# Kernel optimization log

Hardware: AMD Instinct MI355X
Metric: run time of the kernel (lower is better)

Reference implementation:

```python
import jax, jax.numpy as jnp
import numpy as np

D_STATE = 16
DT_RANK = 48
D_CONV = 4
EPS = 1e-5


def rmsnorm(x, w):
    return x * jax.lax.rsqrt(jnp.mean(x * x, axis=-1, keepdims=True) + EPS) * w


def causal_dw_conv(u, w, b):
    # u: [B,T,D], w: [D,K] depthwise causal kernel, b: [D]
    B, T, D = u.shape
    K = w.shape[1]
    up = jnp.pad(u, ((0, 0), (K - 1, 0), (0, 0)))
    acc = jnp.zeros_like(u)
    for k in range(K):  # K=4, tiny fixed loop
        acc = acc + up[:, k:k + T, :] * w[:, k]
    return acc + b


def mamba_mixer(h, ipw, cw, cb, xpw, dpw, dpb, alog, dpar, opw):
    # h: [B,T,d_model]
    B, T, _ = h.shape
    xz = h @ ipw.T                       # [B,T,2*d_inner]
    u, z = jnp.split(xz, 2, axis=-1)     # each [B,T,d_inner]
    u = jax.nn.silu(causal_dw_conv(u, cw, cb))
    xp = u @ xpw.T                       # [B,T,dt_rank+2*d_state]
    dt = xp[..., :DT_RANK]
    Bm = xp[..., DT_RANK:DT_RANK + D_STATE]
    Cm = xp[..., DT_RANK + D_STATE:]
    delta = jax.nn.softplus(dt @ dpw.T + dpb)      # [B,T,d_inner]
    A = -jnp.exp(alog)                              # [d_inner, d_state], negative
    dA = jnp.exp(delta[..., None] * A)              # [B,T,d_inner,d_state] in (0,1)
    dBu = (delta * u)[..., None] * Bm[:, :, None, :]
    # time-major for scan
    dA_t = jnp.moveaxis(dA, 1, 0)
    dBu_t = jnp.moveaxis(dBu, 1, 0)
    C_t = jnp.moveaxis(Cm, 1, 0)

    def step(hst, inp):
        a, bu, c = inp
        hst = a * hst + bu                          # [B,d_inner,d_state]
        y = jnp.einsum('bdn,bn->bd', hst, c)
        return hst, y

    h0 = jnp.zeros((B, u.shape[-1], D_STATE), u.dtype)
    _, ys = jax.lax.scan(step, h0, (dA_t, dBu_t, C_t))
    y = jnp.moveaxis(ys, 0, 1) + u * dpar           # skip via D
    y = y * jax.nn.silu(z)                          # gate
    return y @ opw.T                                # [B,T,d_model]


def setup_inputs() -> dict:
    key = jax.random.key(0)
    ks = jax.random.split(key, 16)
    L, d_model, d_inner = 4, 768, 1536
    B, C, T = 4, 256, 512
    s = 0.02
    return {
        'x': jax.random.normal(ks[0], (B, C, T), jnp.float32),
        'in_proj_w': jax.random.normal(ks[1], (L, 2 * d_inner, d_model), jnp.float32) * s,
        'conv_w': jax.random.normal(ks[2], (L, d_inner, D_CONV), jnp.float32) * 0.3,
        'conv_b': jnp.zeros((L, d_inner), jnp.float32),
        'x_proj_w': jax.random.normal(ks[3], (L, DT_RANK + 2 * D_STATE, d_inner), jnp.float32) * s,
        'dt_proj_w': jax.random.normal(ks[4], (L, d_inner, DT_RANK), jnp.float32) * 0.1,
        'dt_proj_b': jax.random.normal(ks[5], (L, d_inner), jnp.float32) * 0.1 - 4.0,
        'A_log': jax.random.uniform(ks[6], (L, d_inner, D_STATE), jnp.float32, 0.0, 1.5),
        'D_param': jax.random.uniform(ks[7], (L, d_inner), jnp.float32),
        'out_proj_w': jax.random.normal(ks[8], (L, d_model, d_inner), jnp.float32) * s,
        'norm_w': jnp.ones((L, d_model), jnp.float32),
        'norm_f_w': jnp.ones((d_model,), jnp.float32),
        'inp_w': jax.random.normal(ks[9], (d_model, C), jnp.float32) * s,
        'inp_b': jnp.zeros((d_model,), jnp.float32),
        'cls_w': jax.random.normal(ks[10], (10, d_model), jnp.float32) * s,
        'cls_b': jnp.zeros((10,), jnp.float32),
    }


def reference(x, in_proj_w, conv_w, conv_b, x_proj_w, dt_proj_w, dt_proj_b,
              A_log, D_param, out_proj_w, norm_w, norm_f_w,
              inp_w, inp_b, cls_w, cls_b):
    # x: (B, C, T) -> (B, T, C)
    xt = jnp.transpose(x, (0, 2, 1))
    h = xt @ inp_w.T + inp_b                # [B,T,d_model]
    hidden = h
    residual = None
    L = in_proj_w.shape[0]
    for l in range(L):
        residual = hidden if residual is None else hidden + residual
        normed = rmsnorm(residual, norm_w[l])
        hidden = mamba_mixer(normed, in_proj_w[l], conv_w[l], conv_b[l],
                             x_proj_w[l], dt_proj_w[l], dt_proj_b[l],
                             A_log[l], D_param[l], out_proj_w[l])
    residual = hidden + residual
    hidden = rmsnorm(residual, norm_f_w)
    pooled = hidden.mean(axis=1)            # [B,d_model]
    logits = pooled @ cls_w.T + cls_b       # [B,num_labels]
    return logits
```

## Files before the change

### kernel.cpp

```cpp
#include <hip/hip_runtime.h>
#include <math.h>

#define D_MODEL 768
#define D_INNER 1536
#define B_SZ 4
#define T_SZ 512
#define ROWS (B_SZ*T_SZ)
#define XP_N 80
#define CH 32
#define CT 16
#define XS 8
#define XKC (D_INNER/XS)
#define OS 4
#define OKC (D_INNER/OS)
#define MN_OUT (ROWS*768)

typedef __attribute__((ext_vector_type(8))) short bf16x8;
typedef __attribute__((ext_vector_type(4))) float f32x4;

#define GLL(g, l) __builtin_amdgcn_global_load_lds( \
    (const __attribute__((address_space(1))) void*)(g), \
    (__attribute__((address_space(3))) void*)(l), 16, 0, 0)

__device__ __forceinline__ float sigmoidf_(float x){ return 1.0f/(1.0f+__expf(-x)); }
__device__ __forceinline__ float siluf_(float x){ return x*sigmoidf_(x); }
__device__ __forceinline__ unsigned short f2bf(float f){
  unsigned u = __builtin_bit_cast(unsigned, f);
  u = (u + 0x7FFFu + ((u >> 16) & 1u)) >> 16;
  return (unsigned short)u;
}

__global__ __launch_bounds__(256) void gemm_bf16(
    const unsigned short* __restrict__ A, const unsigned short* __restrict__ Wb,
    float* __restrict__ C, int M, int N, int K)
{
  __shared__ unsigned short As[2][64*32];
  __shared__ unsigned short Ws[2][128*32];
  const int tid = threadIdx.x;
  const int bm = blockIdx.y*64, bn = blockIdx.x*128;
  const int wave = tid >> 6, lane = tid & 63;
  const int wn = wave*32;
  const int fr = lane & 15, quad = lane >> 4;
  f32x4 acc[4][2] = {};
  const int chunk = wave*64 + lane;
  const int row0 = chunk >> 2;
  const int khp  = chunk & 3;
  const int khl  = (khp + 4 - ((row0 >> 1) & 3)) & 3;
  const unsigned short* Ag = A  + (size_t)(bm + row0)*K + khl*8;
  const unsigned short* Wg = Wb + (size_t)(bn + row0)*K + khl*8;
  const size_t rstep = (size_t)64*K;
  const int wo = wave*512;

  GLL(Ag,         As[0] + wo);
  GLL(Wg,         Ws[0] + wo);
  GLL(Wg + rstep, Ws[0] + wo + 2048);
  asm volatile("s_waitcnt vmcnt(0)" ::: "memory");
  __builtin_amdgcn_sched_barrier(0);
  __builtin_amdgcn_s_barrier();

  int cur = 0;
  for (int k0 = 0; k0 < K; k0 += 32){
    const int nxt = cur ^ 1;
    if (k0 + 32 < K){
      GLL(Ag + k0 + 32,         As[nxt] + wo);
      GLL(Wg + k0 + 32,         Ws[nxt] + wo);
      GLL(Wg + rstep + k0 + 32, Ws[nxt] + wo + 2048);
    }
    bf16x8 a[4], b[2];
    #pragma unroll
    for (int i=0;i<4;i++){
      const int row = i*16 + fr;
      a[i] = *(const bf16x8*)(As[cur] + row*32 + (((quad + (row>>1)) & 3)*8));
    }
    #pragma unroll
    for (int j=0;j<2;j++){
      const int row = wn + j*16 + fr;
      b[j] = *(const bf16x8*)(Ws[cur] + row*32 + (((quad + (row>>1)) & 3)*8));
    }
    #pragma unroll
    for (int i=0;i<4;i++)
      #pragma unroll
      for (int j=0;j<2;j++)
        acc[i][j] = __builtin_amdgcn_mfma_f32_16x16x32_bf16(a[i], b[j], acc[i][j], 0, 0, 0);
    asm volatile("s_waitcnt vmcnt(0)" ::: "memory");
    __builtin_amdgcn_sched_barrier(0);
    __builtin_amdgcn_s_barrier();
    cur = nxt;
  }
  #pragma unroll
  for (int i=0;i<4;i++){
    #pragma unroll
    for (int r=0;r<4;r++){
      const int row = bm + i*16 + quad*4 + r;
      float* Cp = C + (size_t)row*N + bn + wn + fr;
      #pragma unroll
      for (int j=0;j<2;j++)
        Cp[j*16] = acc[i][j][r];
    }
  }
}

__global__ __launch_bounds__(256) void gemm_bf16_sk(
    const unsigned short* __restrict__ A, const unsigned short* __restrict__ Wb,
    float* __restrict__ P0, float* __restrict__ P1, int M, int N, int K)
{
  __shared__ unsigned short As[2][64*32];
  __shared__ unsigned short Ws[2][128*32];
  const int tid = threadIdx.x;
  const int bm = blockIdx.y*64, bn = blockIdx.x*128;
  const int s = blockIdx.z;
  const int koff = s*OKC;
  const int wave = tid >> 6, lane = tid & 63;
  const int wn = wave*32;
  const int fr = lane & 15, quad = lane >> 4;
  f32x4 acc[4][2] = {};
  const int chunk = wave*64 + lane;
  const int row0 = chunk >> 2;
  const int khp  = chunk & 3;
  const int khl  = (khp + 4 - ((row0 >> 1) & 3)) & 3;
  const unsigned short* Ag = A  + (size_t)(bm + row0)*K + koff + khl*8;
  const unsigned short* Wg = Wb + (size_t)(bn + row0)*K + koff + khl*8;
  const size_t rstep = (size_t)64*K;
  const int wo = wave*512;

  GLL(Ag,         As[0] + wo);
  GLL(Wg,         Ws[0] + wo);
  GLL(Wg + rstep, Ws[0] + wo + 2048);
  asm volatile("s_waitcnt vmcnt(0)" ::: "memory");
  __builtin_amdgcn_sched_barrier(0);
  __builtin_amdgcn_s_barrier();

  int cur = 0;
  for (int k0 = 0; k0 < OKC; k0 += 32){
    const int nxt = cur ^ 1;
    if (k0 + 32 < OKC){
      GLL(Ag + k0 + 32,         As[nxt] + wo);
      GLL(Wg + k0 + 32,         Ws[nxt] + wo);
      GLL(Wg + rstep + k0 + 32, Ws[nxt] + wo + 2048);
    }
    bf16x8 a[4], b[2];
    #pragma unroll
    for (int i=0;i<4;i++){
      const int row = i*16 + fr;
      a[i] = *(const bf16x8*)(As[cur] + row*32 + (((quad + (row>>1)) & 3)*8));
    }
    #pragma unroll
    for (int j=0;j<2;j++){
      const int row = wn + j*16 + fr;
      b[j] = *(const bf16x8*)(Ws[cur] + row*32 + (((quad + (row>>1)) & 3)*8));
    }
    #pragma unroll
    for (int i=0;i<4;i++)
      #pragma unroll
      for (int j=0;j<2;j++)
        acc[i][j] = __builtin_amdgcn_mfma_f32_16x16x32_bf16(a[i], b[j], acc[i][j], 0, 0, 0);
    asm volatile("s_waitcnt vmcnt(0)" ::: "memory");
    __builtin_amdgcn_sched_barrier(0);
    __builtin_amdgcn_s_barrier();
    cur = nxt;
  }
  float* Cb = (s < 2 ? P0 : P1) + (size_t)(s & 1)*MN_OUT;
  #pragma unroll
  for (int i=0;i<4;i++){
    #pragma unroll
    for (int r=0;r<4;r++){
      const int row = bm + i*16 + quad*4 + r;
      float* Cp = Cb + (size_t)row*N + bn + wn + fr;
      #pragma unroll
      for (int j=0;j<2;j++)
        Cp[j*16] = acc[i][j][r];
    }
  }
}

__global__ __launch_bounds__(256) void sgemm_input(
    const float* __restrict__ x, const float* __restrict__ W,
    const float* __restrict__ bias, float* __restrict__ C)
{
  __shared__ float As[16][64];
  __shared__ float Wsh[16][64];
  const int bm = blockIdx.y*64, bn = blockIdx.x*64;
  const int b = bm >> 9, t0 = bm & (T_SZ-1);
  const int tid = threadIdx.x;
  const int tx = tid & 15, ty = tid >> 4;
  const int lm = tid & 63, lk = (tid >> 6) << 2;
  float acc[4][4] = {};
  const float* Wp = W + (size_t)(bn+lm)*256 + lk;
  const float* xb = x + ((size_t)b*256)*512 + t0 + lm;
  for (int k0 = 0; k0 < 256; k0 += 16){
    #pragma unroll
    for (int i=0;i<4;i++)
      As[lk+i][lm] = xb[(size_t)(k0+lk+i)*512];
    float4 wv = *(const float4*)(Wp + k0);
    Wsh[lk+0][lm]=wv.x; Wsh[lk+1][lm]=wv.y; Wsh[lk+2][lm]=wv.z; Wsh[lk+3][lm]=wv.w;
    __syncthreads();
    #pragma unroll
    for (int k = 0; k < 16; k++){
      float a[4], w[4];
      #pragma unroll
      for (int i=0;i<4;i++) a[i] = As[k][ty*4+i];
      #pragma unroll
      for (int j=0;j<4;j++) w[j] = Wsh[k][tx*4+j];
      #pragma unroll
      for (int i=0;i<4;i++)
        #pragma unroll
        for (int j=0;j<4;j++)
          acc[i][j] += a[i]*w[j];
    }
    __syncthreads();
  }
  #pragma unroll
  for (int i=0;i<4;i++){
    const int r = bm + ty*4 + i;
    #pragma unroll
    for (int j=0;j<4;j++){
      const int n = bn + tx*4 + j;
      C[(size_t)r*768 + n] = acc[i][j] + bias[n];
    }
  }
}

__global__ __launch_bounds__(256) void xproj_conv_splitk(
    const float* __restrict__ xz, const float* __restrict__ cw,
    const float* __restrict__ cb, const float* __restrict__ W,
    float* __restrict__ part)
{
  __shared__ float As[16][64];
  __shared__ float Wsh[16][80];
  const int bm = blockIdx.x*64;
  const int s = blockIdx.y;
  const int koff = s*XKC;
  const int tid = threadIdx.x;
  const int tx = tid & 15, ty = tid >> 4;
  const int lm = tid & 63, lk = (tid >> 6) << 2;
  float acc[4][5] = {};
  const int row = bm + lm;
  const int t = row & (T_SZ-1);
  for (int k0 = 0; k0 < XKC; k0 += 16){
    const int d0 = koff + k0 + lk;
    float4 cbv = *(const float4*)(cb + d0);
    float cba[4] = {cbv.x, cbv.y, cbv.z, cbv.w};
    float4 tp3 = *(const float4*)(xz + (size_t)row*3072 + d0);
    float4 tp0 = (t>=3) ? *(const float4*)(xz + (size_t)(row-3)*3072 + d0) : make_float4(0.f,0.f,0.f,0.f);
    float4 tp1 = (t>=2) ? *(const float4*)(xz + (size_t)(row-2)*3072 + d0) : make_float4(0.f,0.f,0.f,0.f);
    float4 tp2 = (t>=1) ? *(const float4*)(xz + (size_t)(row-1)*3072 + d0) : make_float4(0.f,0.f,0.f,0.f);
    float a0[4]={tp0.x,tp0.y,tp0.z,tp0.w}, a1[4]={tp1.x,tp1.y,tp1.z,tp1.w};
    float a2[4]={tp2.x,tp2.y,tp2.z,tp2.w}, a3[4]={tp3.x,tp3.y,tp3.z,tp3.w};
    #pragma unroll
    for (int i=0;i<4;i++){
      const float4 w4 = *(const float4*)(cw + (size_t)(d0+i)*4);
      float a = cba[i];
      a += a0[i]*w4.x; a += a1[i]*w4.y; a += a2[i]*w4.z; a += a3[i]*w4.w;
      As[lk+i][lm] = siluf_(a);
    }
    for (int i = tid; i < 320; i += 256){
      const int wr = i % 80, wk = (i / 80) << 2;
      float4 wv = *(const float4*)(W + (size_t)wr*D_INNER + koff + k0 + wk);
      Wsh[wk+0][wr]=wv.x; Wsh[wk+1][wr]=wv.y; Wsh[wk+2][wr]=wv.z; Wsh[wk+3][wr]=wv.w;
    }
    __syncthreads();
    #pragma unroll
    for (int k = 0; k < 16; k++){
      float a[4], w[5];
      #pragma unroll
      for (int i=0;i<4;i++) a[i] = As[k][ty*4+i];
      #pragma unroll
      for (int j=0;j<5;j++) w[j] = Wsh[k][tx*5+j];
      #pragma unroll
      for (int i=0;i<4;i++)
        #pragma unroll
        for (int j=0;j<5;j++)
          acc[i][j] += a[i]*w[j];
    }
    __syncthreads();
  }
  #pragma unroll
  for (int i=0;i<4;i++){
    const int r = bm + ty*4 + i;
    #pragma unroll
    for (int j=0;j<5;j++){
      const int n = tx*5 + j;
      part[((size_t)s*ROWS + r)*XP_N + n] = acc[i][j];
    }
  }
}

__global__ __launch_bounds__(256) void dtproj_fused(
    const float* __restrict__ part, const float* __restrict__ W,
    const float* __restrict__ bias, float* __restrict__ delta,
    float* __restrict__ xpbc)
{
  if (blockIdx.x >= 24){
    const int i = ((blockIdx.x - 24)*32 + blockIdx.y)*256 + threadIdx.x;
    const int r = i >> 5, cc = i & 31;
    float ssum = 0.f;
    #pragma unroll
    for (int s2=0;s2<XS;s2++)
      ssum += part[((size_t)s2*ROWS + r)*XP_N + 48 + cc];
    xpbc[(size_t)r*32 + cc] = ssum;
    return;
  }
  __shared__ float As[16][64];
  __shared__ float Wsh[16][64];
  const int bm = blockIdx.y*64, bn = blockIdx.x*64;
  const int tid = threadIdx.x;
  const int tx = tid & 15, ty = tid >> 4;
  const int lm = tid & 63, lk = (tid >> 6) << 2;
  float acc[4][4] = {};
  const float* Ap = part + (size_t)(bm+lm)*XP_N + lk;
  const float* Wp = W + (size_t)(bn+lm)*48 + lk;
  for (int k0 = 0; k0 < 48; k0 += 16){
    float4 av = make_float4(0.f,0.f,0.f,0.f);
    #pragma unroll
    for (int s2=0;s2<XS;s2++){
      const float4 pv = *(const float4*)(Ap + (size_t)s2*ROWS*XP_N + k0);
      av.x += pv.x; av.y += pv.y; av.z += pv.z; av.w += pv.w;
    }
    float4 wv = *(const float4*)(Wp + k0);
    As[lk+0][lm]=av.x; As[lk+1][lm]=av.y; As[lk+2][lm]=av.z; As[lk+3][lm]=av.w;
    Wsh[lk+0][lm]=wv.x; Wsh[lk+1][lm]=wv.y; Wsh[lk+2][lm]=wv.z; Wsh[lk+3][lm]=wv.w;
    __syncthreads();
    #pragma unroll
    for (int k = 0; k < 16; k++){
      float a[4], w[4];
      #pragma unroll
      for (int i=0;i<4;i++) a[i] = As[k][ty*4+i];
      #pragma unroll
      for (int j=0;j<4;j++) w[j] = Wsh[k][tx*4+j];
      #pragma unroll
      for (int i=0;i<4;i++)
        #pragma unroll
        for (int j=0;j<4;j++)
          acc[i][j] += a[i]*w[j];
    }
    __syncthreads();
  }
  #pragma unroll
  for (int i=0;i<4;i++){
    const int r = bm + ty*4 + i;
    #pragma unroll
    for (int j=0;j<4;j++){
      const int n = bn + tx*4 + j;
      float v = acc[i][j] + bias[n];
      v = (v > 20.f) ? v : log1pf(__expf(v));
      delta[(size_t)r*D_INNER + n] = v;
    }
  }
}

__global__ __launch_bounds__(256) void scan_pass1(
    const float* __restrict__ delta, const float* __restrict__ xz,
    const float* __restrict__ xpbc, const float* __restrict__ alog,
    const float* __restrict__ cw, const float* __restrict__ cb,
    float* __restrict__ Pend, float* __restrict__ Hend)
{
  const int d = blockIdx.x*256 + threadIdx.x;
  const int b = blockIdx.y, c = blockIdx.z;
  float4 t0 = *(const float4*)(alog + d*16 + 0);
  float4 t1 = *(const float4*)(alog + d*16 + 4);
  float4 t2 = *(const float4*)(alog + d*16 + 8);
  float4 t3 = *(const float4*)(alog + d*16 + 12);
  float Av[16] = {t0.x,t0.y,t0.z,t0.w,t1.x,t1.y,t1.z,t1.w,
                  t2.x,t2.y,t2.z,t2.w,t3.x,t3.y,t3.z,t3.w};
  float h[16];
  #pragma unroll
  for (int n=0;n<16;n++){ Av[n] = -__expf(Av[n]); h[n]=0.f; }
  float sdv = 0.f;
  const size_t row0 = (size_t)b*T_SZ + (size_t)c*CT;
  const float* dp  = delta + row0*D_INNER + d;
  const float* xp0 = xz    + row0*3072 + d;
  const float* bp  = xpbc  + row0*32;
  const float4 cwv = *(const float4*)(cw + (size_t)d*4);
  const float cbv = cb[d];
  float xm3, xm2, xm1;
  if (c == 0){ xm3 = xm2 = xm1 = 0.f; }
  else { xm3 = xp0[-3*3072]; xm2 = xp0[-2*3072]; xm1 = xp0[-1*3072]; }
  #pragma unroll 4
  for (int tt=0; tt<CT; tt++){
    const float dv = dp[(size_t)tt*D_INNER];
    const float xc = xp0[(size_t)tt*3072];
    float ua = cbv;
    ua += xm3*cwv.x; ua += xm2*cwv.y; ua += xm1*cwv.z; ua += xc*cwv.w;
    const float uv = siluf_(ua);
    xm3 = xm2; xm2 = xm1; xm1 = xc;
    const float4 B0 = *(const float4*)(bp + (size_t)tt*32);
    const float4 B1 = *(const float4*)(bp + (size_t)tt*32 + 4);
    const float4 B2 = *(const float4*)(bp + (size_t)tt*32 + 8);
    const float4 B3 = *(const float4*)(bp + (size_t)tt*32 + 12);
    const float Bv[16] = {B0.x,B0.y,B0.z,B0.w,B1.x,B1.y,B1.z,B1.w,
                          B2.x,B2.y,B2.z,B2.w,B3.x,B3.y,B3.z,B3.w};
    const float du = dv*uv;
    sdv += dv;
    #pragma unroll
    for (int n=0;n<16;n++){
      const float dA = __expf(dv*Av[n]);
      h[n] = dA*h[n] + du*Bv[n];
    }
  }
  float P[16];
  #pragma unroll
  for (int n=0;n<16;n++) P[n] = __expf(Av[n]*sdv);
  float* Pp = Pend + ((size_t)(b*CH+c)*D_INNER + d)*16;
  float* Hp = Hend + ((size_t)(b*CH+c)*D_INNER + d)*16;
  *(float4*)(Pp+ 0) = make_float4(P[0],P[1],P[2],P[3]);
  *(float4*)(Pp+ 4) = make_float4(P[4],P[5],P[6],P[7]);
  *(float4*)(Pp+ 8) = make_float4(P[8],P[9],P[10],P[11]);
  *(float4*)(Pp+12) = make_float4(P[12],P[13],P[14],P[15]);
  *(float4*)(Hp+ 0) = make_float4(h[0],h[1],h[2],h[3]);
  *(float4*)(Hp+ 4) = make_float4(h[4],h[5],h[6],h[7]);
  *(float4*)(Hp+ 8) = make_float4(h[8],h[9],h[10],h[11]);
  *(float4*)(Hp+12) = make_float4(h[12],h[13],h[14],h[15]);
}

__global__ __launch_bounds__(256) void scan_combine(
    const float* __restrict__ Pend, const float* __restrict__ Hend,
    float* __restrict__ Hin)
{
  const int gid = blockIdx.x*256 + threadIdx.x;
  const int b = gid / (D_INNER*16);
  const int r = gid % (D_INNER*16);
  const size_t base = (size_t)b*CH*D_INNER*16 + r;
  const size_t step = (size_t)D_INNER*16;
  float h = 0.f;
  Hin[base] = 0.f;
  #pragma unroll
  for (int c=0; c<CH-1; c++){
    h = Pend[base + (size_t)c*step]*h + Hend[base + (size_t)c*step];
    Hin[base + (size_t)(c+1)*step] = h;
  }
}

__global__ __launch_bounds__(256) void scan_pass3(
    const float* __restrict__ delta, const float* __restrict__ xz,
    const float* __restrict__ xpbc, const float* __restrict__ alog,
    const float* __restrict__ cw, const float* __restrict__ cb,
    const float* __restrict__ Dp, const float* __restrict__ Hin,
    unsigned short* __restrict__ yb)
{
  const int d = blockIdx.x*256 + threadIdx.x;
  const int b = blockIdx.y, c = blockIdx.z;
  float4 t0 = *(const float4*)(alog + d*16 + 0);
  float4 t1 = *(const float4*)(alog + d*16 + 4);
  float4 t2 = *(const float4*)(alog + d*16 + 8);
  float4 t3 = *(const float4*)(alog + d*16 + 12);
  float Av[16] = {t0.x,t0.y,t0.z,t0.w,t1.x,t1.y,t1.z,t1.w,
                  t2.x,t2.y,t2.z,t2.w,t3.x,t3.y,t3.z,t3.w};
  #pragma unroll
  for (int n=0;n<16;n++) Av[n] = -__expf(Av[n]);
  const float* Hp = Hin + ((size_t)(b*CH+c)*D_INNER + d)*16;
  float4 h0 = *(const float4*)(Hp+0);
  float4 h1 = *(const float4*)(Hp+4);
  float4 h2 = *(const float4*)(Hp+8);
  float4 h3 = *(const float4*)(Hp+12);
  float h[16] = {h0.x,h0.y,h0.z,h0.w,h1.x,h1.y,h1.z,h1.w,
                 h2.x,h2.y,h2.z,h2.w,h3.x,h3.y,h3.z,h3.w};
  const float Dv = Dp[d];
  const size_t row0 = (size_t)b*T_SZ + (size_t)c*CT;
  const float* dp  = delta + row0*D_INNER + d;
  const float* xp0 = xz    + row0*3072 + d;
  const float* zp  = xz    + row0*3072 + 1536 + d;
  const float* bp  = xpbc  + row0*32;
  unsigned short* yp = yb + row0*D_INNER + d;
  const float4 cwv = *(const float4*)(cw + (size_t)d*4);
  const float cbv = cb[d];
  float xm3, xm2, xm1;
  if (c == 0){ xm3 = xm2 = xm1 = 0.f; }
  else { xm3 = xp0[-3*3072]; xm2 = xp0[-2*3072]; xm1 = xp0[-1*3072]; }
  #pragma unroll 2
  for (int tt=0; tt<CT; tt++){
    const float dv = dp[(size_t)tt*D_INNER];
    const float xc = xp0[(size_t)tt*3072];
    const float zv = zp[(size_t)tt*3072];
    float ua = cbv;
    ua += xm3*cwv.x; ua += xm2*cwv.y; ua += xm1*cwv.z; ua += xc*cwv.w;
    const float uv = siluf_(ua);
    xm3 = xm2; xm2 = xm1; xm1 = xc;
    const float4 B0 = *(const float4*)(bp + (size_t)tt*32);
    const float4 B1 = *(const float4*)(bp + (size_t)tt*32 + 4);
    const float4 B2 = *(const float4*)(bp + (size_t)tt*32 + 8);
    const float4 B3 = *(const float4*)(bp + (size_t)tt*32 + 12);
    const float4 C0 = *(const float4*)(bp + (size_t)tt*32 + 16);
    const float4 C1 = *(const float4*)(bp + (size_t)tt*32 + 20);
    const float4 C2 = *(const float4*)(bp + (size_t)tt*32 + 24);
    const float4 C3 = *(const float4*)(bp + (size_t)tt*32 + 28);
    const float Bv[16] = {B0.x,B0.y,B0.z,B0.w,B1.x,B1.y,B1.z,B1.w,
                          B2.x,B2.y,B2.z,B2.w,B3.x,B3.y,B3.z,B3.w};
    const float Cv[16] = {C0.x,C0.y,C0.z,C0.w,C1.x,C1.y,C1.z,C1.w,
                          C2.x,C2.y,C2.z,C2.w,C3.x,C3.y,C3.z,C3.w};
    const float du = dv*uv;
    float pp = 0.f;
    #pragma unroll
    for (int n=0;n<16;n++){
      const float dA = __expf(dv*Av[n]);
      h[n] = dA*h[n] + du*Bv[n];
      pp += h[n]*Cv[n];
    }
    yp[(size_t)tt*D_INNER] = f2bf((pp + uv*Dv)*siluf_(zv));
  }
}

__global__ __launch_bounds__(256) void fused_norm_cast(
    float* __restrict__ resid, const float* __restrict__ P0, const float* __restrict__ P1,
    const float* __restrict__ w, unsigned short* __restrict__ obf, float* __restrict__ ofp,
    const float* __restrict__ cin1, unsigned short* __restrict__ co1, int cn1, int cnb1,
    const float* __restrict__ cin2, unsigned short* __restrict__ co2, int cn2)
{
  const int blk = blockIdx.x;
  if (blk >= 2048){
    const int cb = blk - 2048;
    const float* in; unsigned short* o; int i4;
    if (cb < cnb1){ in = cin1; o = co1; i4 = (cb*256 + threadIdx.x)*4; if (i4 >= cn1) return; }
    else { in = cin2; o = co2; i4 = ((cb-cnb1)*256 + threadIdx.x)*4; if (i4 >= cn2) return; }
    float4 v = *(const float4*)(in + i4);
    ushort4 r;
    r.x = f2bf(v.x); r.y = f2bf(v.y); r.z = f2bf(v.z); r.w = f2bf(v.w);
    *(ushort4*)(o + i4) = r;
    return;
  }
  const int row = blk;
  const int tid = threadIdx.x;
  float v[3];
  float ss = 0.f;
  #pragma unroll
  for (int i=0;i<3;i++){
    const int c = tid + i*256;
    const size_t idx = (size_t)row*768 + c;
    float r = resid[idx];
    if (P0) r += (P0[idx] + P0[MN_OUT + idx]) + (P1[idx] + P1[MN_OUT + idx]);
    v[i] = r;
    ss += r*r;
  }
  #pragma unroll
  for (int off=32; off>=1; off>>=1) ss += __shfl_xor(ss, off);
  __shared__ float sred[4];
  const int lane = tid & 63, wv = tid >> 6;
  if (lane == 0) sred[wv] = ss;
  __syncthreads();
  const float tot = sred[0]+sred[1]+sred[2]+sred[3];
  const float scale = rsqrtf(tot*(1.0f/768.0f) + 1e-5f);
  #pragma unroll
  for (int i=0;i<3;i++){
    const int c = tid + i*256;
    const size_t idx = (size_t)row*768 + c;
    if (P0) resid[idx] = v[i];
    const float o = v[i]*scale*w[c];
    if (obf) obf[idx] = f2bf(o);
    else     ofp[idx] = o;
  }
}

__global__ __launch_bounds__(256) void pool_partial(const float* __restrict__ normed,
                                                    float* __restrict__ part){
  const int i = blockIdx.x*256 + threadIdx.x;
  const int s = blockIdx.y;
  const int b = i / 768, m = i % 768;
  float sum = 0.f;
  const float* p = normed + ((size_t)b*T_SZ + s*32)*768 + m;
  #pragma unroll
  for (int t=0; t<32; t++) sum += p[(size_t)t*768];
  part[s*3072 + i] = sum;
}

__global__ __launch_bounds__(256) void pool_cls(const float* __restrict__ part,
                                                const float* __restrict__ cw,
                                                const float* __restrict__ cb,
                                                float* __restrict__ out){
  __shared__ float ls[768];
  const int b = blockIdx.x;
  const int tid = threadIdx.x;
  #pragma unroll
  for (int i=0;i<3;i++){
    const int m = tid + i*256;
    float s = 0.f;
    #pragma unroll
    for (int c=0;c<16;c++) s += part[c*3072 + b*768 + m];
    ls[m] = s * (1.0f/T_SZ);
  }
  __syncthreads();
  const int wave = tid >> 6, lane = tid & 63;
  for (int o = wave; o < 10; o += 4){
    float s = 0.f;
    for (int k = lane; k < 768; k += 64) s += ls[k]*cw[o*768 + k];
    #pragma unroll
    for (int off=32; off>=1; off>>=1) s += __shfl_xor(s, off);
    if (lane == 0) out[b*10 + o] = s + cb[o];
  }
}

extern "C" void kernel_launch(void* const* d_in, const int* in_sizes, int n_in,
                              void* d_out, int out_size, void* d_ws, size_t ws_size,
                              hipStream_t stream) {
  const float* x         = (const float*)d_in[0];
  const float* in_proj_w = (const float*)d_in[1];
  const float* conv_w    = (const float*)d_in[2];
  const float* conv_b    = (const float*)d_in[3];
  const float* x_proj_w  = (const float*)d_in[4];
  const float* dt_proj_w = (const float*)d_in[5];
  const float* dt_proj_b = (const float*)d_in[6];
  const float* A_log     = (const float*)d_in[7];
  const float* D_param   = (const float*)d_in[8];
  const float* out_proj_w= (const float*)d_in[9];
  const float* norm_w    = (const float*)d_in[10];
  const float* norm_f_w  = (const float*)d_in[11];
  const float* inp_w     = (const float*)d_in[12];
  const float* inp_b     = (const float*)d_in[13];
  const float* cls_w     = (const float*)d_in[14];
  const float* cls_b     = (const float*)d_in[15];
  float* out = (float*)d_out;

  char* ws = (char*)d_ws;
  auto carve = [&](size_t nelem)->float* {
    float* p = (float*)ws;
    ws += ((nelem*sizeof(float) + 255)/256)*256;
    return p;
  };
  float* resid  = carve((size_t)ROWS*768);
  float* normed = carve((size_t)ROWS*768);
  float* xz     = carve((size_t)ROWS*3072);
  float* ucv    = carve((size_t)ROWS*1536);
  float* xpbc   = carve((size_t)ROWS*32);
  float* delta  = carve((size_t)ROWS*1536);
  float* ybf_f  = carve((size_t)ROWS*1536/2);
  float* wbi_f  = carve((size_t)(3072*768)/2);
  float* wbo_f  = carve((size_t)(768*1536)/2);
  float* Pend   = carve((size_t)B_SZ*CH*D_INNER*16);
  float* Hend   = carve((size_t)B_SZ*CH*D_INNER*16);
  float* Hin    = carve((size_t)B_SZ*CH*D_INNER*16);
  float* xpart  = carve((size_t)XS*ROWS*XP_N);
  float* ppool  = carve((size_t)16*3072);

  unsigned short* normedb = (unsigned short*)normed;
  unsigned short* ybf = (unsigned short*)ybf_f;
  unsigned short* wbi = (unsigned short*)wbi_f;
  unsigned short* wbo = (unsigned short*)wbo_f;

  sgemm_input<<<dim3(12,32), 256, 0, stream>>>(x, inp_w, inp_b, resid);

  for (int l = 0; l < 4; l++){
    fused_norm_cast<<<2048 + 2304 + 1152, 256, 0, stream>>>(
        resid, l ? delta : nullptr, l ? ucv : nullptr,
        norm_w + (size_t)l*768, normedb, nullptr,
        in_proj_w + (size_t)l*3072*768, wbi, 3072*768, 2304,
        out_proj_w + (size_t)l*768*1536, wbo, 768*1536);
    gemm_bf16<<<dim3(24,32), 256, 0, stream>>>(normedb, wbi, xz, ROWS, 3072, 768);
    xproj_conv_splitk<<<dim3(32,XS), 256, 0, stream>>>(
        xz, conv_w + (size_t)l*1536*4, conv_b + (size_t)l*1536,
        x_proj_w + (size_t)l*XP_N*1536, xpart);
    dtproj_fused<<<dim3(32,32), 256, 0, stream>>>(
        xpart, dt_proj_w + (size_t)l*1536*48, dt_proj_b + (size_t)l*1536, delta, xpbc);
    scan_pass1<<<dim3(6,B_SZ,CH-1), 256, 0, stream>>>(
        delta, xz, xpbc, A_log + (size_t)l*1536*16,
        conv_w + (size_t)l*1536*4, conv_b + (size_t)l*1536, Pend, Hend);
    scan_combine<<<(B_SZ*D_INNER*16)/256, 256, 0, stream>>>(Pend, Hend, Hin);
    scan_pass3<<<dim3(6,B_SZ,CH), 256, 0, stream>>>(
        delta, xz, xpbc, A_log + (size_t)l*1536*16,
        conv_w + (size_t)l*1536*4, conv_b + (size_t)l*1536,
        D_param + (size_t)l*1536, Hin, ybf);
    gemm_bf16_sk<<<dim3(6,32,OS), 256, 0, stream>>>(ybf, wbo, delta, ucv, ROWS, 768, 1536);
  }

  fused_norm_cast<<<2048, 256, 0, stream>>>(
      resid, delta, ucv, norm_f_w, nullptr, normed,
      nullptr, nullptr, 0, 0, nullptr, nullptr, 0);
  pool_partial<<<dim3(12,16), 256, 0, stream>>>(normed, ppool);
  pool_cls<<<4, 256, 0, stream>>>(ppool, cls_w, cls_b, out);
}
```

Before: 813.9 us.

## Halve scan chunk count, shrink out-proj split-K, recompute chunk decay in combine

The chunked scan now uses 16 chunks of 32 timesteps instead of 32 of 16. The first pass stores only the per-channel delta sum instead of 16 decay products, and the combine kernel recomputes exp(A*sum) from A_log, which cuts the Pend write and read traffic. Out-proj split-K drops from 4 to 2, so the norm kernel sums two partial buffers instead of four. Fewer chunks mean a longer serial loop per thread and fewer blocks in the scan passes, and the lower split-K means fewer blocks in the out-proj GEMM.

```diff
diff --git a/kernel.cpp b/kernel.cpp
--- a/kernel.cpp
+++ b/kernel.cpp
@@ -7,11 +7,11 @@
 #define T_SZ 512
 #define ROWS (B_SZ*T_SZ)
 #define XP_N 80
-#define CH 32
-#define CT 16
+#define CH 16
+#define CT 32
 #define XS 8
 #define XKC (D_INNER/XS)
-#define OS 4
+#define OS 2
 #define OKC (D_INNER/OS)
 #define MN_OUT (ROWS*768)
 
@@ -159,7 +159,7 @@
     __builtin_amdgcn_s_barrier();
     cur = nxt;
   }
-  float* Cb = (s < 2 ? P0 : P1) + (size_t)(s & 1)*MN_OUT;
+  float* Cb = (s == 0 ? P0 : P1);
   #pragma unroll
   for (int i=0;i<4;i++){
     #pragma unroll
@@ -352,7 +352,7 @@
     const float* __restrict__ delta, const float* __restrict__ xz,
     const float* __restrict__ xpbc, const float* __restrict__ alog,
     const float* __restrict__ cw, const float* __restrict__ cb,
-    float* __restrict__ Pend, float* __restrict__ Hend)
+    float* __restrict__ sdvp, float* __restrict__ Hend)
 {
   const int d = blockIdx.x*256 + threadIdx.x;
   const int b = blockIdx.y, c = blockIdx.z;
@@ -397,15 +397,8 @@
       h[n] = dA*h[n] + du*Bv[n];
     }
   }
-  float P[16];
-  #pragma unroll
-  for (int n=0;n<16;n++) P[n] = __expf(Av[n]*sdv);
-  float* Pp = Pend + ((size_t)(b*CH+c)*D_INNER + d)*16;
+  sdvp[(size_t)(b*CH+c)*D_INNER + d] = sdv;
   float* Hp = Hend + ((size_t)(b*CH+c)*D_INNER + d)*16;
-  *(float4*)(Pp+ 0) = make_float4(P[0],P[1],P[2],P[3]);
-  *(float4*)(Pp+ 4) = make_float4(P[4],P[5],P[6],P[7]);
-  *(float4*)(Pp+ 8) = make_float4(P[8],P[9],P[10],P[11]);
-  *(float4*)(Pp+12) = make_float4(P[12],P[13],P[14],P[15]);
   *(float4*)(Hp+ 0) = make_float4(h[0],h[1],h[2],h[3]);
   *(float4*)(Hp+ 4) = make_float4(h[4],h[5],h[6],h[7]);
   *(float4*)(Hp+ 8) = make_float4(h[8],h[9],h[10],h[11]);
@@ -413,20 +406,25 @@
 }
 
 __global__ __launch_bounds__(256) void scan_combine(
-    const float* __restrict__ Pend, const float* __restrict__ Hend,
-    float* __restrict__ Hin)
+    const float* __restrict__ sdvp, const float* __restrict__ Hend,
+    const float* __restrict__ alog, float* __restrict__ Hin)
 {
   const int gid = blockIdx.x*256 + threadIdx.x;
   const int b = gid / (D_INNER*16);
   const int r = gid % (D_INNER*16);
-  const size_t base = (size_t)b*CH*D_INNER*16 + r;
-  const size_t step = (size_t)D_INNER*16;
+  const int d = r >> 4;
+  const float Av = -__expf(alog[r]);
+  const size_t baseh = (size_t)b*CH*D_INNER*16 + r;
+  const size_t steph = (size_t)D_INNER*16;
+  const size_t bases = (size_t)b*CH*D_INNER + d;
+  const size_t steps = (size_t)D_INNER;
   float h = 0.f;
-  Hin[base] = 0.f;
+  Hin[baseh] = 0.f;
   #pragma unroll
   for (int c=0; c<CH-1; c++){
-    h = Pend[base + (size_t)c*step]*h + Hend[base + (size_t)c*step];
-    Hin[base + (size_t)(c+1)*step] = h;
+    const float P = __expf(Av * sdvp[bases + (size_t)c*steps]);
+    h = P*h + Hend[baseh + (size_t)c*steph];
+    Hin[baseh + (size_t)(c+1)*steph] = h;
   }
 }
 
@@ -526,7 +524,7 @@
     const int c = tid + i*256;
     const size_t idx = (size_t)row*768 + c;
     float r = resid[idx];
-    if (P0) r += (P0[idx] + P0[MN_OUT + idx]) + (P1[idx] + P1[MN_OUT + idx]);
+    if (P0) r += P0[idx] + P1[idx];
     v[i] = r;
     ss += r*r;
   }
@@ -623,7 +621,7 @@
   float* ybf_f  = carve((size_t)ROWS*1536/2);
   float* wbi_f  = carve((size_t)(3072*768)/2);
   float* wbo_f  = carve((size_t)(768*1536)/2);
-  float* Pend   = carve((size_t)B_SZ*CH*D_INNER*16);
+  float* sdvbuf = carve((size_t)B_SZ*CH*D_INNER);
   float* Hend   = carve((size_t)B_SZ*CH*D_INNER*16);
   float* Hin    = carve((size_t)B_SZ*CH*D_INNER*16);
   float* xpart  = carve((size_t)XS*ROWS*XP_N);
@@ -650,8 +648,9 @@
         xpart, dt_proj_w + (size_t)l*1536*48, dt_proj_b + (size_t)l*1536, delta, xpbc);
     scan_pass1<<<dim3(6,B_SZ,CH-1), 256, 0, stream>>>(
         delta, xz, xpbc, A_log + (size_t)l*1536*16,
-        conv_w + (size_t)l*1536*4, conv_b + (size_t)l*1536, Pend, Hend);
-    scan_combine<<<(B_SZ*D_INNER*16)/256, 256, 0, stream>>>(Pend, Hend, Hin);
+        conv_w + (size_t)l*1536*4, conv_b + (size_t)l*1536, sdvbuf, Hend);
+    scan_combine<<<(B_SZ*D_INNER*16)/256, 256, 0, stream>>>(
+        sdvbuf, Hend, A_log + (size_t)l*1536*16, Hin);
     scan_pass3<<<dim3(6,B_SZ,CH), 256, 0, stream>>>(
         delta, xz, xpbc, A_log + (size_t)l*1536*16,
         conv_w + (size_t)l*1536*4, conv_b + (size_t)l*1536,
```

Measured after the change: 821.2 us. No clear change (+0.9%).
